# Kernel optimization log

Hardware: AMD Instinct MI355X
Metric: run time of the kernel (lower is better)

Reference implementation:

```python
import jax, jax.numpy as jnp
import numpy as np

EMBED_DIM = 1024
NUM_HEADS = 16
HEAD_DIM = EMBED_DIM // NUM_HEADS
BATCH = 4
SEQ = 2048


def setup_inputs() -> dict:
    key = jax.random.key(0)
    ks = jax.random.split(key, 9)
    s = 1.0 / np.sqrt(EMBED_DIM)
    return {
        "hidden_states": jax.random.normal(ks[0], (BATCH, SEQ, EMBED_DIM), jnp.float32),
        "Wq": jax.random.normal(ks[1], (EMBED_DIM, EMBED_DIM), jnp.float32) * s,
        "bq": jax.random.normal(ks[2], (EMBED_DIM,), jnp.float32) * s,
        "Wk": jax.random.normal(ks[3], (EMBED_DIM, EMBED_DIM), jnp.float32) * s,
        "bk": jax.random.normal(ks[4], (EMBED_DIM,), jnp.float32) * s,
        "Wv": jax.random.normal(ks[5], (EMBED_DIM, EMBED_DIM), jnp.float32) * s,
        "bv": jax.random.normal(ks[6], (EMBED_DIM,), jnp.float32) * s,
        "Wo": jax.random.normal(ks[7], (EMBED_DIM, EMBED_DIM), jnp.float32) * s,
        "bo": jax.random.normal(ks[8], (EMBED_DIM,), jnp.float32) * s,
        "active_heads": 12,
    }


def reference(hidden_states, Wq, bq, Wk, bk, Wv, bv, Wo, bo, active_heads):
    B, S, E = hidden_states.shape
    H, D = NUM_HEADS, HEAD_DIM
    scale = D ** (-0.5)

    def proj(W, b):  # torch nn.Linear: x @ W.T + b, then split heads -> [B,H,S,D]
        y = jnp.einsum("bse,fe->bsf", hidden_states, W) + b
        return y.reshape(B, S, H, D).transpose(0, 2, 1, 3)

    q, k, v = proj(Wq, bq), proj(Wk, bk), proj(Wv, bv)

    # head_mask built from active_heads (static int): first `active_heads` heads on
    head_mask = (jnp.arange(H) < active_heads).astype(hidden_states.dtype)  # [H]
    hm = head_mask[None, :, None, None]
    q, k, v = q * hm, k * hm, v * hm

    scores = jnp.einsum("bhqd,bhkd->bhqk", q, k) * scale  # [B,H,S,S]
    probs = jax.nn.softmax(scores, axis=-1)
    attn = jnp.einsum("bhqk,bhkd->bhqd", probs, v)  # [B,H,S,D]
    attn = attn.transpose(0, 2, 1, 3).reshape(B, S, E)

    channel_mask = jnp.repeat(head_mask, D)  # [E]
    attn = attn * channel_mask[None, None, :]

    return jnp.einsum("bse,fe->bsf", attn, Wo) + bo
```

## Files before the change

### kernel.cpp

```cpp
#include <hip/hip_runtime.h>
#include <hip/hip_bf16.h>
#include <stdint.h>

#define E_DIM 1024
#define H_NUM 16
#define D_DIM 64
#define B_NUM 4
#define S_LEN 2048
#define M_DIM (B_NUM * S_LEN)
#define KVB 64
#define NT (S_LEN / KVB)

typedef short bf16x8 __attribute__((ext_vector_type(8)));
typedef float f32x4 __attribute__((ext_vector_type(4)));
typedef float f32x16 __attribute__((ext_vector_type(16)));
typedef unsigned short u16;
typedef unsigned int u32;
typedef u16 u16x4 __attribute__((ext_vector_type(4)));
typedef u16 u16x8 __attribute__((ext_vector_type(8)));
typedef u32 u32x2 __attribute__((ext_vector_type(2)));
typedef float fl4 __attribute__((ext_vector_type(4)));

typedef const __attribute__((address_space(1))) void* gas_ptr;
typedef __attribute__((address_space(3))) void* las_ptr;

__device__ __forceinline__ u16 f2bf(float f) {
    uint32_t u = __builtin_bit_cast(uint32_t, f);
    u += 0x7fffu + ((u >> 16) & 1u);
    return (u16)(u >> 16);
}

__device__ __forceinline__ u32 cvtpk(float lo, float hi) {
    u32 r;
    asm("v_cvt_pk_bf16_f32 %0, %1, %2" : "=v"(r) : "v"(lo), "v"(hi));
    return r;
}

__device__ __forceinline__ void gload16(const u16* g, u16* l) {
    __builtin_amdgcn_global_load_lds((gas_ptr)g, (las_ptr)l, 16, 0, 0);
}

__global__ __launch_bounds__(256) void cvt_kernel(const float* __restrict__ in,
                                                  u16* __restrict__ out, int n4) {
    int idx = blockIdx.x * 256 + threadIdx.x;
    int stride = gridDim.x * 256;
    for (int i = idx; i < n4; i += stride) {
        fl4 v = ((const fl4*)in)[i];
        u16x4 o;
#pragma unroll
        for (int j = 0; j < 4; j++) o[j] = f2bf(v[j]);
        ((u16x4*)out)[i] = o;
    }
}

__global__ __launch_bounds__(256) void cvt_w4(const float* __restrict__ w0, const float* __restrict__ w1,
                                              const float* __restrict__ w2, const float* __restrict__ w3,
                                              u16* o0, u16* o1, u16* o2, u16* o3, int n4) {
    const int z = blockIdx.y;
    const float* in = z == 0 ? w0 : (z == 1 ? w1 : (z == 2 ? w2 : w3));
    u16* out = z == 0 ? o0 : (z == 1 ? o1 : (z == 2 ? o2 : o3));
    int idx = blockIdx.x * 256 + threadIdx.x;
    int stride = gridDim.x * 256;
    for (int i = idx; i < n4; i += stride) {
        fl4 v = ((const fl4*)in)[i];
        u16x4 o;
#pragma unroll
        for (int j = 0; j < 4; j++) o[j] = f2bf(v[j]);
        ((u16x4*)out)[i] = o;
    }
}

__device__ __forceinline__ void gemm_loop(const u16* __restrict__ A, const u16* __restrict__ Bw,
                                          int m0, int n0, u16* Ash, u16* Bsh,
                                          f32x4 (&acc)[4][4]) {
    const int t = threadIdx.x, w = t >> 6, lane = t & 63;
    const int li = lane & 15, lg = lane >> 4;
    const int srow = lane >> 2, scol = (lane & 3) * 8;
    const int wr = (w >> 1) * 64, wc = (w & 1) * 64;
    const int K = 1024;

    auto stage = [&](int buf, int k0) {
#pragma unroll
        for (int r = 0; r < 2; r++) {
            int rowbase = r * 64 + w * 16;
            gload16(A + (size_t)(m0 + rowbase + srow) * K + k0 + scol,
                    Ash + buf * 4096 + rowbase * 32);
            gload16(Bw + (size_t)(n0 + rowbase + srow) * K + k0 + scol,
                    Bsh + buf * 4096 + rowbase * 32);
        }
    };

    stage(0, 0);
    asm volatile("s_waitcnt vmcnt(0)" ::: "memory");
    __builtin_amdgcn_s_barrier();
    for (int it = 0; it < 32; ++it) {
        const int cur = it & 1;
        if (it < 31) stage(cur ^ 1, (it + 1) * 32);
        const u16* Ac = Ash + cur * 4096;
        const u16* Bc = Bsh + cur * 4096;
        bf16x8 af[4], bfr[4];
#pragma unroll
        for (int i = 0; i < 4; i++)
            af[i] = *(const bf16x8*)&Ac[(wr + i * 16 + li) * 32 + lg * 8];
#pragma unroll
        for (int j = 0; j < 4; j++)
            bfr[j] = *(const bf16x8*)&Bc[(wc + j * 16 + li) * 32 + lg * 8];
#pragma unroll
        for (int i = 0; i < 4; i++)
#pragma unroll
            for (int j = 0; j < 4; j++)
                acc[i][j] = __builtin_amdgcn_mfma_f32_16x16x32_bf16(af[i], bfr[j], acc[i][j], 0, 0, 0);
        asm volatile("s_waitcnt vmcnt(0)" ::: "memory");
        __builtin_amdgcn_sched_barrier(0);
        __builtin_amdgcn_s_barrier();
    }
}

__device__ __forceinline__ void epi_qk(f32x4 (&acc)[4][4], const float* bias, u16* o,
                                       int m0, int n0) {
    const int t = threadIdx.x, w = t >> 6, lane = t & 63;
    const int li = lane & 15, lg = lane >> 4;
    const int wr = (w >> 1) * 64, wc = (w & 1) * 64;
#pragma unroll
    for (int i = 0; i < 4; i++)
#pragma unroll
        for (int j = 0; j < 4; j++) {
            const int col = n0 + wc + j * 16 + li;
            const float bv = bias[col];
            const int hh = col >> 6, dd = col & 63;
#pragma unroll
            for (int ri = 0; ri < 4; ri++) {
                int row = m0 + wr + i * 16 + lg * 4 + ri;
                int bb = row >> 11, ss = row & 2047;
                o[((size_t)(bb * H_NUM + hh) * S_LEN + ss) * D_DIM + dd] =
                    f2bf(acc[i][j][ri] + bv);
            }
        }
}

__device__ __forceinline__ void epi_vt(f32x4 (&acc)[4][4], const float* bias, u16* o,
                                       int m0, int n0) {
    const int t = threadIdx.x, w = t >> 6, lane = t & 63;
    const int li = lane & 15, lg = lane >> 4;
    const int wr = (w >> 1) * 64, wc = (w & 1) * 64;
#pragma unroll
    for (int i = 0; i < 4; i++)
#pragma unroll
        for (int j = 0; j < 4; j++) {
            const int col = n0 + wc + j * 16 + li;
            const float bv = bias[col];
            const int hh = col >> 6, dd = col & 63;
            int row0 = m0 + wr + i * 16 + lg * 4;
            int bb = row0 >> 11, ss = row0 & 2047;
            u16x4 pk;
#pragma unroll
            for (int ri = 0; ri < 4; ri++) pk[ri] = f2bf(acc[i][j][ri] + bv);
            *(u16x4*)&o[((size_t)(bb * H_NUM + hh) * D_DIM + dd) * S_LEN + ss] = pk;
        }
}

__global__ __launch_bounds__(256) void gemm_qkv(const u16* __restrict__ A,
                                                const u16* __restrict__ W0, const u16* __restrict__ W1,
                                                const u16* __restrict__ W2,
                                                const float* __restrict__ b0, const float* __restrict__ b1,
                                                const float* __restrict__ b2,
                                                u16* Qo, u16* Ko, u16* Vo) {
    __shared__ u16 Ash[2][128 * 32];
    __shared__ u16 Bsh[2][128 * 32];
    const int z = blockIdx.z;
    const u16* Bw = z == 0 ? W0 : (z == 1 ? W1 : W2);
    const float* bias = z == 0 ? b0 : (z == 1 ? b1 : b2);
    const int m0 = blockIdx.y * 128, n0 = blockIdx.x * 128;
    f32x4 acc[4][4] = {};
    gemm_loop(A, Bw, m0, n0, &Ash[0][0], &Bsh[0][0], acc);
    if (z == 0) epi_qk(acc, bias, Qo, m0, n0);
    else if (z == 1) epi_qk(acc, bias, Ko, m0, n0);
    else epi_vt(acc, bias, Vo, m0, n0);
}

__global__ __launch_bounds__(256) void gemm_out(const u16* __restrict__ A, const u16* __restrict__ Bw,
                                                const float* __restrict__ bias, float* __restrict__ o) {
    __shared__ u16 Ash[2][128 * 32];
    __shared__ u16 Bsh[2][128 * 32];
    const int m0 = blockIdx.y * 128, n0 = blockIdx.x * 128;
    f32x4 acc[4][4] = {};
    gemm_loop(A, Bw, m0, n0, &Ash[0][0], &Bsh[0][0], acc);
    const int t = threadIdx.x, w = t >> 6, lane = t & 63;
    const int li = lane & 15, lg = lane >> 4;
    const int wr = (w >> 1) * 64, wc = (w & 1) * 64;
#pragma unroll
    for (int i = 0; i < 4; i++)
#pragma unroll
        for (int j = 0; j < 4; j++) {
            const int col = n0 + wc + j * 16 + li;
            const float bv = bias[col];
#pragma unroll
            for (int ri = 0; ri < 4; ri++) {
                int row = m0 + wr + i * 16 + lg * 4 + ri;
                o[(size_t)row * E_DIM + col] = acc[i][j][ri] + bv;
            }
        }
}

__global__ __launch_bounds__(256) void attn_kernel(const u16* __restrict__ Qg,
                                                   const u16* __restrict__ Kg,
                                                   const u16* __restrict__ Vt,
                                                   u16* __restrict__ attn_out,
                                                   const int* __restrict__ actp) {
    const int bh = blockIdx.y, h = bh & (H_NUM - 1), b = bh >> 4;
    const int t = threadIdx.x, w = t >> 6, lane = t & 63;
    const int ql = lane & 31, hi = lane >> 5;
    const int active = *actp;

    if (h >= active) {
        int row = blockIdx.x * 128 + (t >> 1);
        u16* dst = attn_out + (size_t)(b * S_LEN + row) * E_DIM + h * D_DIM + (t & 1) * 32;
        u16x8 z = {};
        *(u16x8*)(dst + 0) = z;
        *(u16x8*)(dst + 8) = z;
        *(u16x8*)(dst + 16) = z;
        *(u16x8*)(dst + 24) = z;
        return;
    }

    const int q0 = blockIdx.x * 128 + w * 32;
    const size_t hoff = (size_t)(b * H_NUM + h) * S_LEN * D_DIM;
    const u16* Qh = Qg + hoff;
    const u16* Kh = Kg + hoff;
    const u16* Vh = Vt + hoff;

    __shared__ __align__(16) u16 Ksh[2][64 * 64];
    __shared__ __align__(16) u16 Vsh[2][64 * 64];
    __shared__ __align__(16) u16 Pl[4][2048];

    char* Pb = (char*)&Pl[w][0] + ql * 128;
    const int sw = (ql & 7) << 4;

    const int srow0 = t >> 3, scolb = (t & 7) << 4;
    const int sc0 = (scolb ^ ((srow0 & 7) << 4)) >> 1;
    const int srow1 = srow0 + 32;
    const int sc1 = (scolb ^ ((srow1 & 7) << 4)) >> 1;

    auto stage = [&](int buf, int kv0) {
        gload16(Kh + (size_t)(kv0 + srow0) * D_DIM + sc0, &Ksh[buf][t * 8]);
        gload16(Kh + (size_t)(kv0 + srow1) * D_DIM + sc1, &Ksh[buf][2048 + t * 8]);
        gload16(Vh + (size_t)srow0 * S_LEN + kv0 + sc0, &Vsh[buf][t * 8]);
        gload16(Vh + (size_t)srow1 * S_LEN + kv0 + sc1, &Vsh[buf][2048 + t * 8]);
    };

    bf16x8 qf[4];
#pragma unroll
    for (int dch = 0; dch < 4; dch++)
        qf[dch] = *(const bf16x8*)&Qh[(size_t)(q0 + ql) * D_DIM + dch * 16 + hi * 8];

    f32x16 o0 = {}, o1 = {};
    float l_run = 0.f;
    const float Cs = 0.125f * 1.44269504f;
    const float mt = 16.0f * Cs;

    stage(0, 0);
    for (int it = 0; it < NT; ++it) {
        const int cur = it & 1;
        stage(cur ^ 1, ((it + 1) & (NT - 1)) * KVB);
        asm volatile("s_waitcnt vmcnt(4)" ::: "memory");
        __builtin_amdgcn_sched_barrier(0);
        __builtin_amdgcn_s_barrier();

        char* Kc = (char*)&Ksh[cur][0];
        char* Vc = (char*)&Vsh[cur][0];

        f32x16 s0 = {}, s1 = {};
#pragma unroll
        for (int d = 0; d < 4; d++) {
            bf16x8 k0 = *(const bf16x8*)(Kc + ql * 128 + ((d * 32 + hi * 16) ^ sw));
            bf16x8 k1 = *(const bf16x8*)(Kc + (32 + ql) * 128 + ((d * 32 + hi * 16) ^ sw));
            s0 = __builtin_amdgcn_mfma_f32_32x32x16_bf16(k0, qf[d], s0, 0, 0, 0);
            s1 = __builtin_amdgcn_mfma_f32_32x32x16_bf16(k1, qf[d], s1, 0, 0, 0);
        }

        float p0[16], p1[16];
#pragma unroll
        for (int j = 0; j < 16; j++) {
            p0[j] = __builtin_amdgcn_exp2f(__builtin_fmaf(s0[j], Cs, -mt));
            p1[j] = __builtin_amdgcn_exp2f(__builtin_fmaf(s1[j], Cs, -mt));
        }
        u32 pk0[8], pk1[8];
        float ls = 0.f;
#pragma unroll
        for (int i = 0; i < 8; i++) {
            pk0[i] = cvtpk(p0[2 * i], p0[2 * i + 1]);
            pk1[i] = cvtpk(p1[2 * i], p1[2 * i + 1]);
            ls += (p0[2 * i] + p0[2 * i + 1]) + (p1[2 * i] + p1[2 * i + 1]);
        }
        ls += __shfl_xor(ls, 32, 64);
        l_run += ls;

        asm volatile("s_waitcnt lgkmcnt(0)" ::: "memory");
        __builtin_amdgcn_sched_barrier(0);

#pragma unroll
        for (int s = 0; s < 4; s++) {
            u32x2 va = {pk0[2 * s], pk0[2 * s + 1]};
            u32x2 vb = {pk1[2 * s], pk1[2 * s + 1]};
            *(u32x2*)(Pb + ((s * 16 + hi * 8) ^ sw)) = va;
            *(u32x2*)(Pb + ((64 + s * 16 + hi * 8) ^ sw)) = vb;
        }

        asm volatile("s_waitcnt lgkmcnt(0)" ::: "memory");
        __builtin_amdgcn_sched_barrier(0);

#pragma unroll
        for (int c = 0; c < 4; c++) {
            bf16x8 pb = *(const bf16x8*)(Pb + ((c * 32 + hi * 16) ^ sw));
            bf16x8 v0 = *(const bf16x8*)(Vc + ql * 128 + ((c * 32 + hi * 16) ^ sw));
            bf16x8 v1 = *(const bf16x8*)(Vc + (32 + ql) * 128 + ((c * 32 + hi * 16) ^ sw));
            o0 = __builtin_amdgcn_mfma_f32_32x32x16_bf16(v0, pb, o0, 0, 0, 0);
            o1 = __builtin_amdgcn_mfma_f32_32x32x16_bf16(v1, pb, o1, 0, 0, 0);
        }

        __builtin_amdgcn_s_barrier();
    }

    const float inv = 1.0f / l_run;
    u16* dst = attn_out + (size_t)(b * S_LEN + q0 + ql) * E_DIM + h * D_DIM;
#pragma unroll
    for (int g = 0; g < 4; g++) {
        u16x4 w0, w1;
#pragma unroll
        for (int e = 0; e < 4; e++) {
            w0[e] = f2bf(o0[4 * g + e] * inv);
            w1[e] = f2bf(o1[4 * g + e] * inv);
        }
        *(u16x4*)(dst + 8 * g + 4 * hi) = w0;
        *(u16x4*)(dst + 32 + 8 * g + 4 * hi) = w1;
    }
}

extern "C" void kernel_launch(void* const* d_in, const int* in_sizes, int n_in,
                              void* d_out, int out_size, void* d_ws, size_t ws_size,
                              hipStream_t stream) {
    const float* hidden = (const float*)d_in[0];
    const float* Wq = (const float*)d_in[1];
    const float* bq = (const float*)d_in[2];
    const float* Wk = (const float*)d_in[3];
    const float* bk = (const float*)d_in[4];
    const float* Wv = (const float*)d_in[5];
    const float* bv = (const float*)d_in[6];
    const float* Wo = (const float*)d_in[7];
    const float* bo = (const float*)d_in[8];
    const int* act = (const int*)d_in[9];

    u16* ws = (u16*)d_ws;
    u16* Xb = ws;
    u16* Wqb = Xb + 8388608;
    u16* Wkb = Wqb + 1048576;
    u16* Wvb = Wkb + 1048576;
    u16* Wob = Wvb + 1048576;
    u16* Qb = Wob + 1048576;
    u16* Kb = Qb + 8388608;
    u16* Vtb = Kb + 8388608;
    u16* Att = Vtb + 8388608;

    cvt_kernel<<<2048, 256, 0, stream>>>(hidden, Xb, 8388608 / 4);
    cvt_w4<<<dim3(512, 4), 256, 0, stream>>>(Wq, Wk, Wv, Wo, Wqb, Wkb, Wvb, Wob, 1048576 / 4);

    gemm_qkv<<<dim3(8, 64, 3), 256, 0, stream>>>(Xb, Wqb, Wkb, Wvb, bq, bk, bv, Qb, Kb, Vtb);

    attn_kernel<<<dim3(S_LEN / 128, B_NUM * H_NUM), 256, 0, stream>>>(Qb, Kb, Vtb, Att, act);

    gemm_out<<<dim3(8, 64), 256, 0, stream>>>(Att, Wob, bo, (float*)d_out);
}
```

Measured before the change: 225.6 us.

## Remap GEMM blocks per XCD and drop LDS double buffering

The QKV and output GEMMs now launch as 1D grids. Each block index is decoded so that the blocks landing on one XCD share a contiguous range of M tiles, which is meant to improve L2 reuse of the activation rows within that XCD. The GEMM main loop also drops its double-buffered LDS staging in favour of a single buffer with two __syncthreads per k-step. That halves LDS use and may raise occupancy, but global loads no longer overlap with the MFMA compute.

```diff
diff --git a/kernel.cpp b/kernel.cpp
--- a/kernel.cpp
+++ b/kernel.cpp
@@ -79,40 +79,27 @@
     const int wr = (w >> 1) * 64, wc = (w & 1) * 64;
     const int K = 1024;
 
-    auto stage = [&](int buf, int k0) {
+    for (int k0 = 0; k0 < K; k0 += 32) {
 #pragma unroll
         for (int r = 0; r < 2; r++) {
             int rowbase = r * 64 + w * 16;
-            gload16(A + (size_t)(m0 + rowbase + srow) * K + k0 + scol,
-                    Ash + buf * 4096 + rowbase * 32);
-            gload16(Bw + (size_t)(n0 + rowbase + srow) * K + k0 + scol,
-                    Bsh + buf * 4096 + rowbase * 32);
-        }
-    };
-
-    stage(0, 0);
-    asm volatile("s_waitcnt vmcnt(0)" ::: "memory");
-    __builtin_amdgcn_s_barrier();
-    for (int it = 0; it < 32; ++it) {
-        const int cur = it & 1;
-        if (it < 31) stage(cur ^ 1, (it + 1) * 32);
-        const u16* Ac = Ash + cur * 4096;
-        const u16* Bc = Bsh + cur * 4096;
+            gload16(A + (size_t)(m0 + rowbase + srow) * K + k0 + scol, Ash + rowbase * 32);
+            gload16(Bw + (size_t)(n0 + rowbase + srow) * K + k0 + scol, Bsh + rowbase * 32);
+        }
+        __syncthreads();
         bf16x8 af[4], bfr[4];
 #pragma unroll
         for (int i = 0; i < 4; i++)
-            af[i] = *(const bf16x8*)&Ac[(wr + i * 16 + li) * 32 + lg * 8];
+            af[i] = *(const bf16x8*)&Ash[(wr + i * 16 + li) * 32 + lg * 8];
 #pragma unroll
         for (int j = 0; j < 4; j++)
-            bfr[j] = *(const bf16x8*)&Bc[(wc + j * 16 + li) * 32 + lg * 8];
+            bfr[j] = *(const bf16x8*)&Bsh[(wc + j * 16 + li) * 32 + lg * 8];
 #pragma unroll
         for (int i = 0; i < 4; i++)
 #pragma unroll
             for (int j = 0; j < 4; j++)
                 acc[i][j] = __builtin_amdgcn_mfma_f32_16x16x32_bf16(af[i], bfr[j], acc[i][j], 0, 0, 0);
-        asm volatile("s_waitcnt vmcnt(0)" ::: "memory");
-        __builtin_amdgcn_sched_barrier(0);
-        __builtin_amdgcn_s_barrier();
+        __syncthreads();
     }
 }
 
@@ -165,14 +152,18 @@
                                                 const float* __restrict__ b0, const float* __restrict__ b1,
                                                 const float* __restrict__ b2,
                                                 u16* Qo, u16* Ko, u16* Vo) {
-    __shared__ u16 Ash[2][128 * 32];
-    __shared__ u16 Bsh[2][128 * 32];
-    const int z = blockIdx.z;
+    __shared__ u16 Ash[128 * 32];
+    __shared__ u16 Bsh[128 * 32];
+    const int bid = blockIdx.x;
+    const int xcd = bid & 7, slot = bid >> 3;
+    const int zn = slot >> 3, mi = slot & 7;
+    const int m_t = xcd * 8 + mi;
+    const int z = zn >> 3, n_t = zn & 7;
     const u16* Bw = z == 0 ? W0 : (z == 1 ? W1 : W2);
     const float* bias = z == 0 ? b0 : (z == 1 ? b1 : b2);
-    const int m0 = blockIdx.y * 128, n0 = blockIdx.x * 128;
+    const int m0 = m_t * 128, n0 = n_t * 128;
     f32x4 acc[4][4] = {};
-    gemm_loop(A, Bw, m0, n0, &Ash[0][0], &Bsh[0][0], acc);
+    gemm_loop(A, Bw, m0, n0, Ash, Bsh, acc);
     if (z == 0) epi_qk(acc, bias, Qo, m0, n0);
     else if (z == 1) epi_qk(acc, bias, Ko, m0, n0);
     else epi_vt(acc, bias, Vo, m0, n0);
@@ -180,11 +171,15 @@
 
 __global__ __launch_bounds__(256) void gemm_out(const u16* __restrict__ A, const u16* __restrict__ Bw,
                                                 const float* __restrict__ bias, float* __restrict__ o) {
-    __shared__ u16 Ash[2][128 * 32];
-    __shared__ u16 Bsh[2][128 * 32];
-    const int m0 = blockIdx.y * 128, n0 = blockIdx.x * 128;
+    __shared__ u16 Ash[128 * 32];
+    __shared__ u16 Bsh[128 * 32];
+    const int bid = blockIdx.x;
+    const int xcd = bid & 7, slot = bid >> 3;
+    const int n_t = slot >> 3, mi = slot & 7;
+    const int m_t = xcd * 8 + mi;
+    const int m0 = m_t * 128, n0 = n_t * 128;
     f32x4 acc[4][4] = {};
-    gemm_loop(A, Bw, m0, n0, &Ash[0][0], &Bsh[0][0], acc);
+    gemm_loop(A, Bw, m0, n0, Ash, Bsh, acc);
     const int t = threadIdx.x, w = t >> 6, lane = t & 63;
     const int li = lane & 15, lg = lane >> 4;
     const int wr = (w >> 1) * 64, wc = (w & 1) * 64;
@@ -364,9 +359,9 @@
     cvt_kernel<<<2048, 256, 0, stream>>>(hidden, Xb, 8388608 / 4);
     cvt_w4<<<dim3(512, 4), 256, 0, stream>>>(Wq, Wk, Wv, Wo, Wqb, Wkb, Wvb, Wob, 1048576 / 4);
 
-    gemm_qkv<<<dim3(8, 64, 3), 256, 0, stream>>>(Xb, Wqb, Wkb, Wvb, bq, bk, bv, Qb, Kb, Vtb);
+    gemm_qkv<<<1536, 256, 0, stream>>>(Xb, Wqb, Wkb, Wvb, bq, bk, bv, Qb, Kb, Vtb);
 
     attn_kernel<<<dim3(S_LEN / 128, B_NUM * H_NUM), 256, 0, stream>>>(Qb, Kb, Vtb, Att, act);
 
-    gemm_out<<<dim3(8, 64), 256, 0, stream>>>(Att, Wob, bo, (float*)d_out);
-}
+    gemm_out<<<512, 256, 0, stream>>>(Att, Wob, bo, (float*)d_out);
+}
```

After: 199.5 us. 1.13x faster.
